# Performance work log

Measured on AMD Instinct MI355X. Metric: run time of the kernel, lower is better.

Reference implementation:

```python
import jax, jax.numpy as jnp
import numpy as np

N = 100000      # total nodes
G = 500         # graphs
NPG = 200       # nodes per graph
E = 1_600_000   # edges
XS = 128        # input feature dim
FIX = 10        # fixed_size one-hot id dim
H = 64          # hidden (neuron)
NPERM = 3
YS = 1


def setup_inputs() -> dict:
    key = jax.random.key(0)
    ks = jax.random.split(key, 10)
    x = jax.random.normal(ks[0], (N, XS), jnp.float32)

    rng = np.random.default_rng(0)
    src = rng.integers(0, N, E)
    off = rng.integers(1, NPG, E)
    dst = (src // NPG) * NPG + (src % NPG + off) % NPG  # edges stay within graph
    edge_index = jnp.asarray(np.stack([src, dst]).astype(np.int32))
    batch_ids = jnp.asarray((np.arange(N) // NPG).astype(np.int32))

    # permuted tiled-eye node ids: node at local pos p gets one_hot(perm[p] % 10)
    base = np.arange(NPG) % FIX  # tiled eye row indices for one graph
    ids = rng.permuted(np.tile(base, (NPERM, G, 1)), axis=-1).reshape(NPERM, N)
    perm_ids = jax.nn.one_hot(jnp.asarray(ids), FIX, dtype=jnp.float32)

    def lin(k, fin, fout):
        return jax.random.normal(k, (fin, fout), jnp.float32) * (1.0 / np.sqrt(fin))

    return {
        "x": x, "edge_index": edge_index, "batch_ids": batch_ids, "perm_ids": perm_ids,
        "w1": lin(ks[1], XS + FIX, H), "b1": jnp.zeros((H,), jnp.float32),
        "w2": lin(ks[2], H, H), "b2": jnp.zeros((H,), jnp.float32),
        "w3": lin(ks[3], H, H), "b3": jnp.zeros((H,), jnp.float32),
        "a1w": lin(ks[4], H, 16), "a1b": jnp.zeros((16,), jnp.float32),
        "a2w": lin(ks[5], 16, YS), "a2b": jnp.zeros((YS,), jnp.float32),
    }


def reference(x, edge_index, batch_ids, perm_ids,
              w1, b1, w2, b2, w3, b3, a1w, a1b, a2w, a2b):
    src, dst = edge_index[0], edge_index[1]
    loop = jnp.arange(N, dtype=src.dtype)
    src_a = jnp.concatenate([src, loop])  # GCNConv adds self-loops
    dst_a = jnp.concatenate([dst, loop])
    deg = jax.ops.segment_sum(jnp.ones_like(dst_a, x.dtype), dst_a, N)
    dinv = jnp.where(deg > 0, deg ** -0.5, 0.0)
    norm = (dinv[src_a] * dinv[dst_a])[:, None]  # [E+N, 1]

    def conv(h, W, b):
        h = h @ W  # transform first (cheaper: H <= in_dim)
        return jax.ops.segment_sum(h[src_a] * norm, dst_a, N) + b

    counts = jnp.maximum(jax.ops.segment_sum(jnp.ones((N,), x.dtype), batch_ids, G), 1.0)

    out = jnp.zeros((G, H), x.dtype)
    for p in range(NPERM):
        h = jnp.concatenate([x, perm_ids[p]], axis=1)  # [N, XS+FIX]
        h = jax.nn.relu(conv(h, w1, b1))
        h = jax.nn.relu(conv(h, w2, b2))
        h = jax.nn.relu(conv(h, w3, b3))
        hg = jax.ops.segment_sum(h, batch_ids, G) / counts[:, None]  # mean pool
        out = out + hg / NPERM

    out = jax.nn.relu(out @ a1w + a1b)
    return out @ a2w + a2b  # [G, YS]
```

## Files before the change

### kernel.cpp

```cpp
#include <hip/hip_runtime.h>

#define NN   100000
#define EE   1600000
#define GG   500
#define NPGc 200
#define HH   64
#define NPERMc 3
#define C1   16384
#define HST  74
#define TST  226

typedef __fp16   h16x2 __attribute__((ext_vector_type(2)));
typedef _Float16 f16x8 __attribute__((ext_vector_type(8)));
typedef float    f32x4 __attribute__((ext_vector_type(4)));

__global__ __launch_bounds__(512) void k_gec(const int* __restrict__ ei, int* __restrict__ gec) {
    __shared__ int h[GG];
    int t = threadIdx.x;
    int base = blockIdx.x * C1;
    int nE = min(C1, EE - base);
    for (int i = t; i < GG; i += 512) h[i] = 0;
    __syncthreads();
    for (int i = t; i < nE; i += 512) {
        int d = ei[EE + base + i];
        atomicAdd(&h[d / NPGc], 1);
    }
    __syncthreads();
    for (int g = t; g < GG; g += 512) if (h[g]) atomicAdd(&gec[g], h[g]);
}

__global__ __launch_bounds__(512) void k_scan500(const int* __restrict__ gec,
                                                 int* __restrict__ goff, int* __restrict__ gcur) {
    __shared__ int sc[512], hh[512];
    int t = threadIdx.x;
    int v = (t < GG) ? gec[t] : 0;
    hh[t] = v; sc[t] = v;
    __syncthreads();
    for (int off = 1; off < 512; off <<= 1) {
        int u = (t >= off) ? sc[t - off] : 0;
        __syncthreads();
        sc[t] += u;
        __syncthreads();
    }
    int excl = sc[t] - hh[t];
    if (t <= GG) goff[t] = excl;
    if (t < GG)  gcur[t] = excl;
}

__global__ __launch_bounds__(512) void k_stage1(const int* __restrict__ ei, int* __restrict__ gcur,
                                                unsigned short* __restrict__ gtok) {
    __shared__ unsigned short stag[C1];
    __shared__ int h[512], esc[512], cur[512], gb[512];
    int t = threadIdx.x;
    int base = blockIdx.x * C1;
    int nE = min(C1, EE - base);
    h[t] = 0; cur[t] = 0;
    __syncthreads();
    for (int i = t; i < nE; i += 512) {
        int s = ei[base + i];
        atomicAdd(&h[s / NPGc], 1);
    }
    __syncthreads();
    esc[t] = h[t];
    __syncthreads();
    for (int off = 1; off < 512; off <<= 1) {
        int u = (t >= off) ? esc[t - off] : 0;
        __syncthreads();
        esc[t] += u;
        __syncthreads();
    }
    esc[t] -= h[t];
    if (t < GG && h[t] > 0) gb[t] = atomicAdd(&gcur[t], h[t]);
    __syncthreads();
    for (int i = t; i < nE; i += 512) {
        int s = ei[base + i], d = ei[EE + base + i];
        int g = s / NPGc;
        int ls = s - g * NPGc, ld = d - g * NPGc;
        int pos = esc[g] + atomicAdd(&cur[g], 1);
        stag[pos] = (unsigned short)(ls | (ld << 8));
    }
    __syncthreads();
    int w = t >> 6, lane = t & 63;
    for (int g = w; g < GG; g += 8) {
        int c = h[g]; if (!c) continue;
        int lb = esc[g], b0 = gb[g];
        for (int j = lane; j < c; j += 64) gtok[b0 + j] = stag[lb + j];
    }
}

__global__ __launch_bounds__(256) void k_wprep(const float* __restrict__ w1,
                                               const float* __restrict__ w2,
                                               const float* __restrict__ w3,
                                               _Float16* __restrict__ wf) {
    int tid = blockIdx.x * 256 + threadIdx.x;
    if (tid >= 64 * 64) return;
    int c = tid >> 6, lane = tid & 63;
    int q = lane >> 4, m = lane & 15;
    const float* src; int kstep, ct, term;
    if (c < 32) { kstep = c & 3; ct = (c >> 2) & 3; term = c >> 4; src = w1; }
    else {
        int c2 = c - 32;
        kstep = c2 & 1; ct = (c2 >> 1) & 3; term = (c2 >> 3) & 1;
        src = (c2 >> 4) ? w3 : w2;
    }
    f16x8 v;
#pragma unroll
    for (int j = 0; j < 8; ++j) {
        int k = kstep * 32 + q * 8 + j;
        int n = ct * 16 + m;
        float wv = src[k * 64 + n];
        _Float16 hi = (_Float16)wv;
        float lo = wv - (float)hi;
        v[j] = term ? (_Float16)lo : hi;
    }
    *((f16x8*)(wf + c * 512) + lane) = v;
}

__device__ __forceinline__ void cvt_hilo(f32x4 a, f32x4 b, f16x8& hi, f16x8& lo) {
    float f[8] = {a[0], a[1], a[2], a[3], b[0], b[1], b[2], b[3]};
#pragma unroll
    for (int j = 0; j < 8; j += 2) {
        h16x2 h = __builtin_amdgcn_cvt_pkrtz(f[j], f[j + 1]);
        h16x2 l = __builtin_amdgcn_cvt_pkrtz(f[j] - (float)h[0], f[j + 1] - (float)h[1]);
        hi[j] = (_Float16)h[0]; hi[j + 1] = (_Float16)h[1];
        lo[j] = (_Float16)l[0]; lo[j + 1] = (_Float16)l[1];
    }
}

__global__ __launch_bounds__(256) void k_xw(const float* __restrict__ x,
                                            const _Float16* __restrict__ wf,
                                            float* __restrict__ xW) {
    int lane = threadIdx.x & 63, w = threadIdx.x >> 6;
    int rbase = blockIdx.x * 64 + w * 16;
    int m = lane & 15, q = lane >> 4;
    int row = rbase + m;
    int rowc = min(row, NN - 1);
    f16x8 Ah[4], Al[4];
#pragma unroll
    for (int ks = 0; ks < 4; ++ks) {
        const float* ar = x + (size_t)rowc * 128 + ks * 32 + q * 8;
        f32x4 f0 = *(const f32x4*)ar;
        f32x4 f1 = *(const f32x4*)(ar + 4);
        cvt_hilo(f0, f1, Ah[ks], Al[ks]);
    }
#pragma unroll
    for (int ct = 0; ct < 4; ++ct) {
        f32x4 acc = {0.f, 0.f, 0.f, 0.f};
#pragma unroll
        for (int ks = 0; ks < 4; ++ks) {
            f16x8 Bh = *((const f16x8*)(wf + ((0 * 4 + ct) * 4 + ks) * 512) + lane);
            f16x8 Bl = *((const f16x8*)(wf + ((1 * 4 + ct) * 4 + ks) * 512) + lane);
            acc = __builtin_amdgcn_mfma_f32_16x16x32_f16(Ah[ks], Bh, acc, 0, 0, 0);
            acc = __builtin_amdgcn_mfma_f32_16x16x32_f16(Al[ks], Bh, acc, 0, 0, 0);
            acc = __builtin_amdgcn_mfma_f32_16x16x32_f16(Ah[ks], Bl, acc, 0, 0, 0);
        }
#pragma unroll
        for (int i = 0; i < 4; ++i) {
            int r = rbase + q * 4 + i;
            if (r < NN) xW[(size_t)r * 64 + ct * 16 + m] = acc[i];
        }
    }
}

__device__ __forceinline__ f16x8 cvt_a8(uint2 v) {
    f16x8 r;
#pragma unroll
    for (int k = 0; k < 4; ++k) r[k] = (_Float16)(float)((v.x >> (8 * k)) & 255u);
#pragma unroll
    for (int k = 0; k < 4; ++k) r[4 + k] = (_Float16)(float)((v.y >> (8 * k)) & 255u);
    return r;
}

template <bool POOL>
__device__ __forceinline__ void conv_mfma(const float* __restrict__ Tt, float* __restrict__ H,
                                          const f16x8 (&Af)[2][7], int w, int m, int q, int nmt,
                                          const float (&dvv)[2][4], const float (&bias)[4],
                                          float (&poolv)[4]) {
    f32x4 acc[2][4];
#pragma unroll
    for (int mi = 0; mi < 2; ++mi)
#pragma unroll
        for (int ct = 0; ct < 4; ++ct) acc[mi][ct] = (f32x4){0.f, 0.f, 0.f, 0.f};

    for (int ks = 0; ks < 7; ++ks) {
#pragma unroll
        for (int ct = 0; ct < 4; ++ct) {
            const float* bp = Tt + (ct * 16 + m) * TST + ks * 32 + q * 8;
            float2 u0 = *(const float2*)bp;
            float2 u1 = *(const float2*)(bp + 2);
            float2 u2 = *(const float2*)(bp + 4);
            float2 u3 = *(const float2*)(bp + 6);
            f32x4 a = {u0.x, u0.y, u1.x, u1.y};
            f32x4 b = {u2.x, u2.y, u3.x, u3.y};
            f16x8 Bh, Bl;
            cvt_hilo(a, b, Bh, Bl);
            acc[0][ct] = __builtin_amdgcn_mfma_f32_16x16x32_f16(Af[0][ks], Bh, acc[0][ct], 0, 0, 0);
            acc[0][ct] = __builtin_amdgcn_mfma_f32_16x16x32_f16(Af[0][ks], Bl, acc[0][ct], 0, 0, 0);
            if (nmt > 1) {
                acc[1][ct] = __builtin_amdgcn_mfma_f32_16x16x32_f16(Af[1][ks], Bh, acc[1][ct], 0, 0, 0);
                acc[1][ct] = __builtin_amdgcn_mfma_f32_16x16x32_f16(Af[1][ks], Bl, acc[1][ct], 0, 0, 0);
            }
        }
    }
#pragma unroll
    for (int mi = 0; mi < 2; ++mi) {
        if (mi >= nmt) break;
        int rbase = (w + 8 * mi) * 16 + q * 4;
#pragma unroll
        for (int ct = 0; ct < 4; ++ct) {
            if (!POOL) {
#pragma unroll
                for (int i = 0; i < 4; ++i)
                    H[(rbase + i) * HST + ct * 16 + m] =
                        fmaxf(fmaf(dvv[mi][i], acc[mi][ct][i], bias[ct]), 0.f);
            } else {
                float pl = 0.f;
#pragma unroll
                for (int i = 0; i < 4; ++i) {
                    float o = fmaxf(fmaf(dvv[mi][i], acc[mi][ct][i], bias[ct]), 0.f);
                    if (rbase + i < NPGc) pl += o;
                }
                poolv[ct] += pl;
            }
        }
    }
}

__device__ __forceinline__ void gemm_mfma(const float* __restrict__ H, float* __restrict__ Tt,
                                          const _Float16* __restrict__ wf, int w, int lane,
                                          int m, int q, int nmt, const float (&dvv)[2][4]) {
#pragma unroll
    for (int mi = 0; mi < 2; ++mi) {
        if (mi >= nmt) break;
        int mt = w + 8 * mi;
        f16x8 Ah[2], Al[2];
#pragma unroll
        for (int ks = 0; ks < 2; ++ks) {
            const float* ap = H + (mt * 16 + m) * HST + ks * 32 + 8 * q;
            float2 u0 = *(const float2*)ap;
            float2 u1 = *(const float2*)(ap + 2);
            float2 u2 = *(const float2*)(ap + 4);
            float2 u3 = *(const float2*)(ap + 6);
            f32x4 a = {u0.x, u0.y, u1.x, u1.y};
            f32x4 b = {u2.x, u2.y, u3.x, u3.y};
            cvt_hilo(a, b, Ah[ks], Al[ks]);
        }
#pragma unroll
        for (int ct = 0; ct < 4; ++ct) {
            f32x4 acc = {0.f, 0.f, 0.f, 0.f};
#pragma unroll
            for (int ks = 0; ks < 2; ++ks) {
                f16x8 Bh = *((const f16x8*)(wf + ((0 * 4 + ct) * 2 + ks) * 512) + lane);
                f16x8 Bl = *((const f16x8*)(wf + ((1 * 4 + ct) * 2 + ks) * 512) + lane);
                acc = __builtin_amdgcn_mfma_f32_16x16x32_f16(Ah[ks], Bh, acc, 0, 0, 0);
                acc = __builtin_amdgcn_mfma_f32_16x16x32_f16(Al[ks], Bh, acc, 0, 0, 0);
                acc = __builtin_amdgcn_mfma_f32_16x16x32_f16(Ah[ks], Bl, acc, 0, 0, 0);
            }
            int off = (ct * 16 + m) * TST + mt * 16 + q * 4;
            *(float2*)(Tt + off)     = make_float2(acc[0] * dvv[mi][0], acc[1] * dvv[mi][1]);
            *(float2*)(Tt + off + 2) = make_float2(acc[2] * dvv[mi][2], acc[3] * dvv[mi][3]);
        }
    }
}

__global__ __launch_bounds__(512, 2) void k_fused(
    const float* __restrict__ xW, const float* __restrict__ perm,
    const float* __restrict__ w1tail,
    const float* __restrict__ b1, const float* __restrict__ b2, const float* __restrict__ b3,
    const _Float16* __restrict__ wsW23,
    const int* __restrict__ goff, const unsigned short* __restrict__ gtok,
    float* __restrict__ gout) {
    __shared__ __align__(16) float smem[15392 + 14464];
    __shared__ __align__(16) _Float16 wlds[16384];
    __shared__ float w1r[640];
    __shared__ float dv[224];
    __shared__ float pool[8 * 64];
    __shared__ int idsl[672];

    unsigned char* A8 = (unsigned char*)smem;
    unsigned int*  A32 = (unsigned int*)smem;
    float* H  = smem;
    float* Tt = smem + 15392;

    int g = blockIdx.x, t = threadIdx.x;
    int lane = t & 63, w = t >> 6;
    int m = lane & 15, q = lane >> 4;
    int nbase = g * NPGc;
    int goffg = goff[g], cnt = goff[g + 1] - goffg;

    for (int i = t; i < 2048; i += 512) ((f16x8*)wlds)[i] = ((const f16x8*)wsW23)[i];
    for (int i = t; i < 640; i += 512) w1r[i] = w1tail[i];
    for (int i = t; i < 11648; i += 512) A32[i] = 0;
    __syncthreads();
    for (int i = t; i < cnt; i += 512) {
        int tok = gtok[goffg + i];
        int addr = (tok >> 8) * 224 + (tok & 255);
        atomicAdd(&A32[addr >> 2], 1u << ((addr & 3) * 8));
    }
    if (t < NPGc) { int a = t * 225; atomicAdd(&A32[a >> 2], 1u << ((a & 3) * 8)); }
    for (int i = t; i < 672; i += 512) {
        int p = i / 224, nd = i - p * 224;
        int id = 0;
        if (nd < NPGc) {
            const float* pp = perm + ((size_t)p * NN + nbase + nd) * 10;
            float best = pp[0];
#pragma unroll
            for (int k = 1; k < 10; ++k) { float v = pp[k]; if (v > best) { best = v; id = k; } }
        }
        idsl[i] = id;
    }
    __syncthreads();
    if (t < 224) {
        unsigned s = 0;
        for (int i = 0; i < 56; ++i) {
            unsigned v = A32[t * 56 + i];
            s += (v & 255u) + ((v >> 8) & 255u) + ((v >> 16) & 255u) + (v >> 24);
        }
        dv[t] = s ? rsqrtf((float)s) : 0.f;
    }
    int nmt = (w < 5) ? 2 : 1;
    f16x8 Af[2][7];
#pragma unroll
    for (int mi = 0; mi < 2; ++mi) {
        int mt = w + 8 * mi;
        if (mt < 13) {
#pragma unroll
            for (int ks = 0; ks < 7; ++ks) {
                uint2 v = *(const uint2*)(A8 + (mt * 16 + m) * 224 + ks * 32 + q * 8);
                Af[mi][ks] = cvt_a8(v);
            }
        }
    }
    __syncthreads();

    float dvv[2][4];
#pragma unroll
    for (int mi = 0; mi < 2; ++mi)
#pragma unroll
        for (int i = 0; i < 4; ++i) {
            int r = (w + 8 * mi) * 16 + q * 4 + i;
            dvv[mi][i] = (w + 8 * mi < 13) ? dv[r] : 0.f;
        }
    float bb1[4], bb2[4], bb3[4];
#pragma unroll
    for (int ct = 0; ct < 4; ++ct) {
        bb1[ct] = b1[ct * 16 + m]; bb2[ct] = b2[ct * 16 + m]; bb3[ct] = b3[ct * 16 + m];
    }

    float poolv[4] = {0.f, 0.f, 0.f, 0.f};

    for (int p = 0; p < NPERMc; ++p) {
        for (int nd = w; nd < 224; nd += 8) {
            float val = 0.f;
            if (nd < NPGc) {
                int id = idsl[p * 224 + nd];
                val = dv[nd] * (xW[(size_t)(nbase + nd) * 64 + lane] + w1r[id * 64 + lane]);
            }
            Tt[lane * TST + nd] = val;
        }
        __syncthreads();
        conv_mfma<false>(Tt, H, Af, w, m, q, nmt, dvv, bb1, poolv);
        __syncthreads();
        gemm_mfma(H, Tt, wlds, w, lane, m, q, nmt, dvv);
        __syncthreads();
        conv_mfma<false>(Tt, H, Af, w, m, q, nmt, dvv, bb2, poolv);
        __syncthreads();
        gemm_mfma(H, Tt, wlds + 8192, w, lane, m, q, nmt, dvv);
        __syncthreads();
        conv_mfma<true>(Tt, H, Af, w, m, q, nmt, dvv, bb3, poolv);
        __syncthreads();
    }

#pragma unroll
    for (int ct = 0; ct < 4; ++ct) {
        float v = poolv[ct];
        v += __shfl_xor(v, 16);
        v += __shfl_xor(v, 32);
        if (q == 0) pool[w * 64 + ct * 16 + m] = v;
    }
    __syncthreads();
    if (w == 0) {
        float tot = 0.f;
#pragma unroll
        for (int i = 0; i < 8; ++i) tot += pool[i * 64 + lane];
        gout[g * 64 + lane] = tot * (1.0f / (NPGc * NPERMc));
    }
}

__global__ __launch_bounds__(64) void k_head(const float* __restrict__ gout, const float* __restrict__ a1w,
                                             const float* __restrict__ a1b, const float* __restrict__ a2w,
                                             const float* __restrict__ a2b, float* __restrict__ out) {
    __shared__ float v[64];
    __shared__ float h[16];
    int g = blockIdx.x, j = threadIdx.x;
    v[j] = gout[g * 64 + j];
    __syncthreads();
    if (j < 16) {
        float a = a1b[j];
        for (int k = 0; k < 64; ++k) a = fmaf(v[k], a1w[k * 16 + j], a);
        h[j] = fmaxf(a, 0.f);
    }
    __syncthreads();
    if (j == 0) {
        float o = a2b[0];
#pragma unroll
        for (int i = 0; i < 16; ++i) o = fmaf(h[i], a2w[i], o);
        out[g] = o;
    }
}


static inline size_t alignup(size_t x) { return (x + 255) & ~(size_t)255; }

extern "C" void kernel_launch(void* const* d_in, const int* in_sizes, int n_in,
                              void* d_out, int out_size, void* d_ws, size_t ws_size,
                              hipStream_t stream) {
    const float* x    = (const float*)d_in[0];
    const int*   ei   = (const int*)d_in[1];
    const float* perm = (const float*)d_in[3];
    const float* w1   = (const float*)d_in[4];
    const float* b1   = (const float*)d_in[5];
    const float* w2   = (const float*)d_in[6];
    const float* b2   = (const float*)d_in[7];
    const float* w3   = (const float*)d_in[8];
    const float* b3   = (const float*)d_in[9];
    const float* a1w  = (const float*)d_in[10];
    const float* a1b  = (const float*)d_in[11];
    const float* a2w  = (const float*)d_in[12];
    const float* a2b  = (const float*)d_in[13];
    float* out = (float*)d_out;

    char* p = (char*)d_ws;
    auto take = [&](size_t bytes) { char* r = p; p += alignup(bytes); return r; };
    float*          xW   = (float*)take((size_t)NN * 64 * 4);
    unsigned short* gtok = (unsigned short*)take((size_t)EE * 2);
    int*            goff = (int*)take(512 * 4);
    int*            gcur = (int*)take(512 * 4);
    float*          gout = (float*)take((size_t)GG * 64 * 4);
    _Float16*       wsW  = (_Float16*)take((size_t)64 * 512 * 2);
    int*            gec  = (int*)take(512 * 4);
    (void)hipMemsetAsync(gec, 0, 512 * 4, stream);

    const int EB = (EE + C1 - 1) / C1;

    k_gec<<<EB, 512, 0, stream>>>(ei, gec);
    k_scan500<<<1, 512, 0, stream>>>(gec, goff, gcur);
    k_stage1<<<EB, 512, 0, stream>>>(ei, gcur, gtok);

    k_wprep<<<16, 256, 0, stream>>>(w1, w2, w3, wsW);
    k_xw<<<(NN + 63) / 64, 256, 0, stream>>>(x, wsW, xW);

    k_fused<<<GG, 512, 0, stream>>>(xW, perm, w1 + 128 * 64, b1, b2, b3,
                                    wsW + 32 * 512, goff, gtok, gout);

    k_head<<<GG, 64, 0, stream>>>(gout, a1w, a1b, a2w, a2b, out);
}
```

Measured before the change: 319.7 us.

## Prepack conv operands as fp16 hi/lo fragments and merge prep/head kernels

Measured after the change: 277.4 us. 1.15x faster.

```diff
diff --git a/kernel.cpp b/kernel.cpp
--- a/kernel.cpp
+++ b/kernel.cpp
@@ -8,58 +8,71 @@
 #define NPERMc 3
 #define C1   16384
 #define HST  74
-#define TST  226
+#define BSTRIDE 4096
 
 typedef __fp16   h16x2 __attribute__((ext_vector_type(2)));
+typedef _Float16 f16x4 __attribute__((ext_vector_type(4)));
 typedef _Float16 f16x8 __attribute__((ext_vector_type(8)));
 typedef float    f32x4 __attribute__((ext_vector_type(4)));
 
-__global__ __launch_bounds__(512) void k_gec(const int* __restrict__ ei, int* __restrict__ gec) {
-    __shared__ int h[GG];
+__device__ __forceinline__ void cvt_hilo(f32x4 a, f32x4 b, f16x8& hi, f16x8& lo) {
+    float f[8] = {a[0], a[1], a[2], a[3], b[0], b[1], b[2], b[3]};
+#pragma unroll
+    for (int j = 0; j < 8; j += 2) {
+        h16x2 h = __builtin_amdgcn_cvt_pkrtz(f[j], f[j + 1]);
+        h16x2 l = __builtin_amdgcn_cvt_pkrtz(f[j] - (float)h[0], f[j + 1] - (float)h[1]);
+        hi[j] = (_Float16)h[0]; hi[j + 1] = (_Float16)h[1];
+        lo[j] = (_Float16)l[0]; lo[j + 1] = (_Float16)l[1];
+    }
+}
+
+__device__ __forceinline__ void cvt_hilo4(const float (&v)[4], f16x4& hv, f16x4& lv) {
+#pragma unroll
+    for (int i = 0; i < 4; i += 2) {
+        h16x2 h = __builtin_amdgcn_cvt_pkrtz(v[i], v[i + 1]);
+        h16x2 l = __builtin_amdgcn_cvt_pkrtz(v[i] - (float)h[0], v[i + 1] - (float)h[1]);
+        hv[i] = (_Float16)h[0]; hv[i + 1] = (_Float16)h[1];
+        lv[i] = (_Float16)l[0]; lv[i + 1] = (_Float16)l[1];
+    }
+}
+
+#define EB 98
+__global__ __launch_bounds__(512) void k_prep(const int* __restrict__ ei, int* __restrict__ gcnt,
+                                              unsigned short* __restrict__ gtok,
+                                              const float* __restrict__ w1, const float* __restrict__ w2,
+                                              const float* __restrict__ w3, _Float16* __restrict__ wf) {
     int t = threadIdx.x;
-    int base = blockIdx.x * C1;
-    int nE = min(C1, EE - base);
-    for (int i = t; i < GG; i += 512) h[i] = 0;
-    __syncthreads();
-    for (int i = t; i < nE; i += 512) {
-        int d = ei[EE + base + i];
-        atomicAdd(&h[d / NPGc], 1);
-    }
-    __syncthreads();
-    for (int g = t; g < GG; g += 512) if (h[g]) atomicAdd(&gec[g], h[g]);
-}
-
-__global__ __launch_bounds__(512) void k_scan500(const int* __restrict__ gec,
-                                                 int* __restrict__ goff, int* __restrict__ gcur) {
-    __shared__ int sc[512], hh[512];
-    int t = threadIdx.x;
-    int v = (t < GG) ? gec[t] : 0;
-    hh[t] = v; sc[t] = v;
-    __syncthreads();
-    for (int off = 1; off < 512; off <<= 1) {
-        int u = (t >= off) ? sc[t - off] : 0;
-        __syncthreads();
-        sc[t] += u;
-        __syncthreads();
-    }
-    int excl = sc[t] - hh[t];
-    if (t <= GG) goff[t] = excl;
-    if (t < GG)  gcur[t] = excl;
-}
-
-__global__ __launch_bounds__(512) void k_stage1(const int* __restrict__ ei, int* __restrict__ gcur,
-                                                unsigned short* __restrict__ gtok) {
+    if (blockIdx.x >= EB) {
+        int tid = (blockIdx.x - EB) * 512 + t;
+        int c = tid >> 6, lane = tid & 63;
+        int q = lane >> 4, m = lane & 15;
+        const float* src; int kstep, ct, term;
+        if (c < 32) { kstep = c & 3; ct = (c >> 2) & 3; term = c >> 4; src = w1; }
+        else {
+            int c2 = c - 32;
+            kstep = c2 & 1; ct = (c2 >> 1) & 3; term = (c2 >> 3) & 1;
+            src = (c2 >> 4) ? w3 : w2;
+        }
+        f16x8 v;
+#pragma unroll
+        for (int j = 0; j < 8; ++j) {
+            int k = kstep * 32 + q * 8 + j;
+            int n = ct * 16 + m;
+            float wv = src[k * 64 + n];
+            _Float16 hi = (_Float16)wv;
+            float lo = wv - (float)hi;
+            v[j] = term ? (_Float16)lo : hi;
+        }
+        *((f16x8*)(wf + c * 512) + lane) = v;
+        return;
+    }
     __shared__ unsigned short stag[C1];
     __shared__ int h[512], esc[512], cur[512], gb[512];
-    int t = threadIdx.x;
     int base = blockIdx.x * C1;
     int nE = min(C1, EE - base);
     h[t] = 0; cur[t] = 0;
     __syncthreads();
-    for (int i = t; i < nE; i += 512) {
-        int s = ei[base + i];
-        atomicAdd(&h[s / NPGc], 1);
-    }
+    for (int i = t; i < nE; i += 512) atomicAdd(&h[ei[base + i] / NPGc], 1);
     __syncthreads();
     esc[t] = h[t];
     __syncthreads();
@@ -70,7 +83,7 @@
         __syncthreads();
     }
     esc[t] -= h[t];
-    if (t < GG && h[t] > 0) gb[t] = atomicAdd(&gcur[t], h[t]);
+    if (t < GG && h[t] > 0) gb[t] = atomicAdd(&gcnt[t], h[t]);
     __syncthreads();
     for (int i = t; i < nE; i += 512) {
         int s = ei[base + i], d = ei[EE + base + i];
@@ -83,47 +96,9 @@
     int w = t >> 6, lane = t & 63;
     for (int g = w; g < GG; g += 8) {
         int c = h[g]; if (!c) continue;
-        int lb = esc[g], b0 = gb[g];
-        for (int j = lane; j < c; j += 64) gtok[b0 + j] = stag[lb + j];
-    }
-}
-
-__global__ __launch_bounds__(256) void k_wprep(const float* __restrict__ w1,
-                                               const float* __restrict__ w2,
-                                               const float* __restrict__ w3,
-                                               _Float16* __restrict__ wf) {
-    int tid = blockIdx.x * 256 + threadIdx.x;
-    if (tid >= 64 * 64) return;
-    int c = tid >> 6, lane = tid & 63;
-    int q = lane >> 4, m = lane & 15;
-    const float* src; int kstep, ct, term;
-    if (c < 32) { kstep = c & 3; ct = (c >> 2) & 3; term = c >> 4; src = w1; }
-    else {
-        int c2 = c - 32;
-        kstep = c2 & 1; ct = (c2 >> 1) & 3; term = (c2 >> 3) & 1;
-        src = (c2 >> 4) ? w3 : w2;
-    }
-    f16x8 v;
-#pragma unroll
-    for (int j = 0; j < 8; ++j) {
-        int k = kstep * 32 + q * 8 + j;
-        int n = ct * 16 + m;
-        float wv = src[k * 64 + n];
-        _Float16 hi = (_Float16)wv;
-        float lo = wv - (float)hi;
-        v[j] = term ? (_Float16)lo : hi;
-    }
-    *((f16x8*)(wf + c * 512) + lane) = v;
-}
-
-__device__ __forceinline__ void cvt_hilo(f32x4 a, f32x4 b, f16x8& hi, f16x8& lo) {
-    float f[8] = {a[0], a[1], a[2], a[3], b[0], b[1], b[2], b[3]};
-#pragma unroll
-    for (int j = 0; j < 8; j += 2) {
-        h16x2 h = __builtin_amdgcn_cvt_pkrtz(f[j], f[j + 1]);
-        h16x2 l = __builtin_amdgcn_cvt_pkrtz(f[j] - (float)h[0], f[j + 1] - (float)h[1]);
-        hi[j] = (_Float16)h[0]; hi[j + 1] = (_Float16)h[1];
-        lo[j] = (_Float16)l[0]; lo[j + 1] = (_Float16)l[1];
+        int lb = esc[g], off = gb[g];
+        int lim = min(c, BSTRIDE - off);
+        for (int j = lane; j < lim; j += 64) gtok[(size_t)g * BSTRIDE + off + j] = stag[lb + j];
     }
 }
 
@@ -172,7 +147,9 @@
 }
 
 template <bool POOL>
-__device__ __forceinline__ void conv_mfma(const float* __restrict__ Tt, float* __restrict__ H,
+__device__ __forceinline__ void conv_mfma(const _Float16* __restrict__ Tfh,
+                                          const _Float16* __restrict__ Tfl,
+                                          float* __restrict__ H,
                                           const f16x8 (&Af)[2][7], int w, int m, int q, int nmt,
                                           const float (&dvv)[2][4], const float (&bias)[4],
                                           float (&poolv)[4]) {
@@ -181,19 +158,12 @@
     for (int mi = 0; mi < 2; ++mi)
 #pragma unroll
         for (int ct = 0; ct < 4; ++ct) acc[mi][ct] = (f32x4){0.f, 0.f, 0.f, 0.f};
-
+    int lane = m + 16 * q;
     for (int ks = 0; ks < 7; ++ks) {
 #pragma unroll
         for (int ct = 0; ct < 4; ++ct) {
-            const float* bp = Tt + (ct * 16 + m) * TST + ks * 32 + q * 8;
-            float2 u0 = *(const float2*)bp;
-            float2 u1 = *(const float2*)(bp + 2);
-            float2 u2 = *(const float2*)(bp + 4);
-            float2 u3 = *(const float2*)(bp + 6);
-            f32x4 a = {u0.x, u0.y, u1.x, u1.y};
-            f32x4 b = {u2.x, u2.y, u3.x, u3.y};
-            f16x8 Bh, Bl;
-            cvt_hilo(a, b, Bh, Bl);
+            f16x8 Bh = *((const f16x8*)(Tfh + (ks * 4 + ct) * 512) + lane);
+            f16x8 Bl = *((const f16x8*)(Tfl + (ks * 4 + ct) * 512) + lane);
             acc[0][ct] = __builtin_amdgcn_mfma_f32_16x16x32_f16(Af[0][ks], Bh, acc[0][ct], 0, 0, 0);
             acc[0][ct] = __builtin_amdgcn_mfma_f32_16x16x32_f16(Af[0][ks], Bl, acc[0][ct], 0, 0, 0);
             if (nmt > 1) {
@@ -226,7 +196,8 @@
     }
 }
 
-__device__ __forceinline__ void gemm_mfma(const float* __restrict__ H, float* __restrict__ Tt,
+__device__ __forceinline__ void gemm_mfma(const float* __restrict__ H,
+                                          _Float16* __restrict__ Tfh, _Float16* __restrict__ Tfl,
                                           const _Float16* __restrict__ wf, int w, int lane,
                                           int m, int q, int nmt, const float (&dvv)[2][4]) {
 #pragma unroll
@@ -245,6 +216,9 @@
             f32x4 b = {u2.x, u2.y, u3.x, u3.y};
             cvt_hilo(a, b, Ah[ks], Al[ks]);
         }
+        int quad = ((mt & 1) << 1) + (q >> 1);
+        int j0 = (q & 1) << 2;
+        int lanep = m + (quad << 4);
 #pragma unroll
         for (int ct = 0; ct < 4; ++ct) {
             f32x4 acc = {0.f, 0.f, 0.f, 0.f};
@@ -256,9 +230,14 @@
                 acc = __builtin_amdgcn_mfma_f32_16x16x32_f16(Al[ks], Bh, acc, 0, 0, 0);
                 acc = __builtin_amdgcn_mfma_f32_16x16x32_f16(Ah[ks], Bl, acc, 0, 0, 0);
             }
-            int off = (ct * 16 + m) * TST + mt * 16 + q * 4;
-            *(float2*)(Tt + off)     = make_float2(acc[0] * dvv[mi][0], acc[1] * dvv[mi][1]);
-            *(float2*)(Tt + off + 2) = make_float2(acc[2] * dvv[mi][2], acc[3] * dvv[mi][3]);
+            float o[4];
+#pragma unroll
+            for (int i = 0; i < 4; ++i) o[i] = acc[i] * dvv[mi][i];
+            f16x4 hv, lv;
+            cvt_hilo4(o, hv, lv);
+            int off = ((mt >> 1) * 4 + ct) * 512 + lanep * 8 + j0;
+            *(f16x4*)(Tfh + off) = hv;
+            *(f16x4*)(Tfl + off) = lv;
         }
     }
 }
@@ -268,33 +247,36 @@
     const float* __restrict__ w1tail,
     const float* __restrict__ b1, const float* __restrict__ b2, const float* __restrict__ b3,
     const _Float16* __restrict__ wsW23,
-    const int* __restrict__ goff, const unsigned short* __restrict__ gtok,
-    float* __restrict__ gout) {
-    __shared__ __align__(16) float smem[15392 + 14464];
+    const int* __restrict__ gcnt, const unsigned short* __restrict__ gtok,
+    const float* __restrict__ a1w, const float* __restrict__ a1b,
+    const float* __restrict__ a2w, const float* __restrict__ a2b,
+    float* __restrict__ out) {
+    __shared__ __align__(16) float Hm[15392];
+    __shared__ __align__(16) _Float16 Tfh[28 * 512];
+    __shared__ __align__(16) _Float16 Tfl[28 * 512];
     __shared__ __align__(16) _Float16 wlds[16384];
     __shared__ float w1r[640];
     __shared__ float dv[224];
     __shared__ float pool[8 * 64];
-    __shared__ int idsl[672];
-
-    unsigned char* A8 = (unsigned char*)smem;
-    unsigned int*  A32 = (unsigned int*)smem;
-    float* H  = smem;
-    float* Tt = smem + 15392;
+    __shared__ unsigned char idsl[672];
+
+    unsigned char* A8  = (unsigned char*)Hm;
+    unsigned int*  A32 = (unsigned int*)Hm;
 
     int g = blockIdx.x, t = threadIdx.x;
     int lane = t & 63, w = t >> 6;
     int m = lane & 15, q = lane >> 4;
     int nbase = g * NPGc;
-    int goffg = goff[g], cnt = goff[g + 1] - goffg;
+    int cnt = min(gcnt[g], BSTRIDE);
+    const unsigned short* tok = gtok + (size_t)g * BSTRIDE;
 
     for (int i = t; i < 2048; i += 512) ((f16x8*)wlds)[i] = ((const f16x8*)wsW23)[i];
     for (int i = t; i < 640; i += 512) w1r[i] = w1tail[i];
-    for (int i = t; i < 11648; i += 512) A32[i] = 0;
+    for (int i = t; i < 2912; i += 512) ((uint4*)A8)[i] = make_uint4(0, 0, 0, 0);
     __syncthreads();
     for (int i = t; i < cnt; i += 512) {
-        int tok = gtok[goffg + i];
-        int addr = (tok >> 8) * 224 + (tok & 255);
+        int tk = tok[i];
+        int addr = (tk >> 8) * 224 + (tk & 255);
         atomicAdd(&A32[addr >> 2], 1u << ((addr & 3) * 8));
     }
     if (t < NPGc) { int a = t * 225; atomicAdd(&A32[a >> 2], 1u << ((a & 3) * 8)); }
@@ -307,15 +289,16 @@
 #pragma unroll
             for (int k = 1; k < 10; ++k) { float v = pp[k]; if (v > best) { best = v; id = k; } }
         }
-        idsl[i] = id;
+        idsl[i] = (unsigned char)id;
     }
     __syncthreads();
     if (t < 224) {
         unsigned s = 0;
-        for (int i = 0; i < 56; ++i) {
-            unsigned v = A32[t * 56 + i];
-            s += (v & 255u) + ((v >> 8) & 255u) + ((v >> 16) & 255u) + (v >> 24);
-        }
+        if (t < 208)
+            for (int i = 0; i < 56; ++i) {
+                unsigned v = A32[t * 56 + i];
+                s += (v & 255u) + ((v >> 8) & 255u) + ((v >> 16) & 255u) + (v >> 24);
+            }
         dv[t] = s ? rsqrtf((float)s) : 0.f;
     }
     int nmt = (w < 5) ? 2 : 1;
@@ -350,24 +333,39 @@
     float poolv[4] = {0.f, 0.f, 0.f, 0.f};
 
     for (int p = 0; p < NPERMc; ++p) {
-        for (int nd = w; nd < 224; nd += 8) {
-            float val = 0.f;
-            if (nd < NPGc) {
-                int id = idsl[p * 224 + nd];
-                val = dv[nd] * (xW[(size_t)(nbase + nd) * 64 + lane] + w1r[id * 64 + lane]);
-            }
-            Tt[lane * TST + nd] = val;
-        }
-        __syncthreads();
-        conv_mfma<false>(Tt, H, Af, w, m, q, nmt, dvv, bb1, poolv);
-        __syncthreads();
-        gemm_mfma(H, Tt, wlds, w, lane, m, q, nmt, dvv);
-        __syncthreads();
-        conv_mfma<false>(Tt, H, Af, w, m, q, nmt, dvv, bb2, poolv);
-        __syncthreads();
-        gemm_mfma(H, Tt, wlds + 8192, w, lane, m, q, nmt, dvv);
-        __syncthreads();
-        conv_mfma<true>(Tt, H, Af, w, m, q, nmt, dvv, bb3, poolv);
+        {
+            const unsigned char* ids = idsl + p * 224;
+            for (int nd0 = w * 28; nd0 < w * 28 + 28; nd0 += 4) {
+                float vals[4];
+#pragma unroll
+                for (int i = 0; i < 4; ++i) {
+                    int nd = nd0 + i;
+                    float v = 0.f;
+                    if (nd < NPGc) {
+                        int id = ids[nd];
+                        v = dv[nd] * (xW[(size_t)(nbase + nd) * 64 + lane] + w1r[id * 64 + lane]);
+                    }
+                    vals[i] = v;
+                }
+                f16x4 hv, lv;
+                cvt_hilo4(vals, hv, lv);
+                int c = (nd0 >> 5) * 4 + (lane >> 4);
+                int lanep = (lane & 15) + (((nd0 & 31) >> 3) << 4);
+                int off = c * 512 + lanep * 8 + (nd0 & 7);
+                *(f16x4*)(Tfh + off) = hv;
+                *(f16x4*)(Tfl + off) = lv;
+            }
+        }
+        __syncthreads();
+        conv_mfma<false>(Tfh, Tfl, Hm, Af, w, m, q, nmt, dvv, bb1, poolv);
+        __syncthreads();
+        gemm_mfma(Hm, Tfh, Tfl, wlds, w, lane, m, q, nmt, dvv);
+        __syncthreads();
+        conv_mfma<false>(Tfh, Tfl, Hm, Af, w, m, q, nmt, dvv, bb2, poolv);
+        __syncthreads();
+        gemm_mfma(Hm, Tfh, Tfl, wlds + 8192, w, lane, m, q, nmt, dvv);
+        __syncthreads();
+        conv_mfma<true>(Tfh, Tfl, Hm, Af, w, m, q, nmt, dvv, bb3, poolv);
         __syncthreads();
     }
 
@@ -379,32 +377,23 @@
         if (q == 0) pool[w * 64 + ct * 16 + m] = v;
     }
     __syncthreads();
-    if (w == 0) {
+    if (t < 64) {
         float tot = 0.f;
 #pragma unroll
-        for (int i = 0; i < 8; ++i) tot += pool[i * 64 + lane];
-        gout[g * 64 + lane] = tot * (1.0f / (NPGc * NPERMc));
-    }
-}
-
-__global__ __launch_bounds__(64) void k_head(const float* __restrict__ gout, const float* __restrict__ a1w,
-                                             const float* __restrict__ a1b, const float* __restrict__ a2w,
-                                             const float* __restrict__ a2b, float* __restrict__ out) {
-    __shared__ float v[64];
-    __shared__ float h[16];
-    int g = blockIdx.x, j = threadIdx.x;
-    v[j] = gout[g * 64 + j];
-    __syncthreads();
-    if (j < 16) {
-        float a = a1b[j];
-        for (int k = 0; k < 64; ++k) a = fmaf(v[k], a1w[k * 16 + j], a);
-        h[j] = fmaxf(a, 0.f);
-    }
-    __syncthreads();
-    if (j == 0) {
+        for (int i = 0; i < 8; ++i) tot += pool[i * 64 + t];
+        pool[t] = tot * (1.0f / (NPGc * NPERMc));
+    }
+    __syncthreads();
+    if (t < 16) {
+        float a = a1b[t];
+        for (int k = 0; k < 64; ++k) a = fmaf(pool[k], a1w[k * 16 + t], a);
+        pool[64 + t] = fmaxf(a, 0.f);
+    }
+    __syncthreads();
+    if (t == 0) {
         float o = a2b[0];
 #pragma unroll
-        for (int i = 0; i < 16; ++i) o = fmaf(h[i], a2w[i], o);
+        for (int i = 0; i < 16; ++i) o = fmaf(pool[64 + i], a2w[i], o);
         out[g] = o;
     }
 }
@@ -433,25 +422,14 @@
     char* p = (char*)d_ws;
     auto take = [&](size_t bytes) { char* r = p; p += alignup(bytes); return r; };
     float*          xW   = (float*)take((size_t)NN * 64 * 4);
-    unsigned short* gtok = (unsigned short*)take((size_t)EE * 2);
-    int*            goff = (int*)take(512 * 4);
-    int*            gcur = (int*)take(512 * 4);
-    float*          gout = (float*)take((size_t)GG * 64 * 4);
+    unsigned short* gtok = (unsigned short*)take((size_t)GG * BSTRIDE * 2);
     _Float16*       wsW  = (_Float16*)take((size_t)64 * 512 * 2);
-    int*            gec  = (int*)take(512 * 4);
-    (void)hipMemsetAsync(gec, 0, 512 * 4, stream);
-
-    const int EB = (EE + C1 - 1) / C1;
-
-    k_gec<<<EB, 512, 0, stream>>>(ei, gec);
-    k_scan500<<<1, 512, 0, stream>>>(gec, goff, gcur);
-    k_stage1<<<EB, 512, 0, stream>>>(ei, gcur, gtok);
-
-    k_wprep<<<16, 256, 0, stream>>>(w1, w2, w3, wsW);
+    int*            gcnt = (int*)take(512 * 4);
+    (void)hipMemsetAsync(gcnt, 0, 512 * 4, stream);
+
+    k_prep<<<EB + 8, 512, 0, stream>>>(ei, gcnt, gtok, w1, w2, w3, wsW);
     k_xw<<<(NN + 63) / 64, 256, 0, stream>>>(x, wsW, xW);
-
     k_fused<<<GG, 512, 0, stream>>>(xW, perm, w1 + 128 * 64, b1, b2, b3,
-                                    wsW + 32 * 512, goff, gtok, gout);
-
-    k_head<<<GG, 64, 0, stream>>>(gout, a1w, a1b, a2w, a2b, out);
-}
+                                    wsW + 32 * 512, gcnt, gtok,
+                                    a1w, a1b, a2w, a2b, out);
+}
```
